# Optimization experiments

Measured on AMD Instinct MI355X. Metric: run time of the kernel, lower is better.

The kernel has to match this reference:

```python
import jax, jax.numpy as jnp
import numpy as np

N = 50000
E = 800000
IN_DIM = 128
HID = 256


def _sage_conv(x, src, dst, W_l, b_l, W_r, num_nodes):
    # PyG SAGEConv (aggr='mean'): out = lin_l(mean_{j in N(i)} x_j) + lin_r(x_i)
    msgs = x[src]                                   # [E, D] gather of source feats
    agg = jax.ops.segment_sum(msgs, dst, num_segments=num_nodes)   # [N, D]
    deg = jax.ops.segment_sum(jnp.ones((src.shape[0],), dtype=x.dtype), dst,
                              num_segments=num_nodes)              # [N]
    agg = agg / jnp.maximum(deg, 1.0)[:, None]      # mean aggregation
    return agg @ W_l + b_l + x @ W_r


def setup_inputs() -> dict:
    key = jax.random.key(0)
    k = jax.random.split(key, 8)
    x = jax.random.normal(k[0], (N, IN_DIM), dtype=jnp.float32)
    edge_index = jax.random.randint(k[1], (2, E), 0, N, dtype=jnp.int64)
    s1 = 1.0 / np.sqrt(IN_DIM)
    s2 = 1.0 / np.sqrt(HID)
    W1_l = jax.random.uniform(k[2], (IN_DIM, HID), jnp.float32, -s1, s1)
    b1 = jax.random.uniform(k[3], (HID,), jnp.float32, -s1, s1)
    W1_r = jax.random.uniform(k[4], (IN_DIM, HID), jnp.float32, -s1, s1)
    W2_l = jax.random.uniform(k[5], (HID, HID), jnp.float32, -s2, s2)
    b2 = jax.random.uniform(k[6], (HID,), jnp.float32, -s2, s2)
    W2_r = jax.random.uniform(k[7], (HID, HID), jnp.float32, -s2, s2)
    return {"x": x, "edge_index": edge_index,
            "W1_l": W1_l, "b1": b1, "W1_r": W1_r,
            "W2_l": W2_l, "b2": b2, "W2_r": W2_r}


def reference(x, edge_index, W1_l, b1, W1_r, W2_l, b2, W2_r):
    src, dst = edge_index[0], edge_index[1]
    h = _sage_conv(x, src, dst, W1_l, b1, W1_r, N)   # [N, HID]
    h = jax.nn.relu(h)
    # dropout is identity in eval mode
    out = _sage_conv(h, src, dst, W2_l, b2, W2_r, N)  # [N, HID]
    return out
```

## Files before the change

### kernel.cpp

```cpp
#include <hip/hip_runtime.h>
#include <hip/hip_bf16.h>


typedef __attribute__((ext_vector_type(8))) short bf16x8;
typedef __attribute__((ext_vector_type(4))) float f32x4;
typedef __attribute__((ext_vector_type(4))) short s16x4;

constexpr int HIDC = 256;

__device__ __forceinline__ short f2bf(float v) {
  __hip_bfloat16 h = __float2bfloat16(v);
  return *reinterpret_cast<short*>(&h);
}
__device__ __forceinline__ float bf2f(short s) {
  unsigned int u = ((unsigned int)(unsigned short)s) << 16;
  float f;
  __builtin_memcpy(&f, &u, 4);
  return f;
}

__device__ __forceinline__ void gll16(const short* g, short* l) {
  __builtin_amdgcn_global_load_lds(
      (const __attribute__((address_space(1))) unsigned int*)g,
      (__attribute__((address_space(3))) unsigned int*)l, 16, 0, 0);
}

__global__ __launch_bounds__(256) void deg_rank_kernel(
    const int* __restrict__ dst, int* __restrict__ deg, int* __restrict__ rank,
    int E, int N) {
  int e = blockIdx.x * blockDim.x + threadIdx.x;
  if (e < E) {
    int d = dst[e];
    if ((unsigned)d < (unsigned)N) rank[e] = atomicAdd(&deg[d], 1);
  }
}

__global__ __launch_bounds__(256) void blocksum_kernel(
    const int* __restrict__ deg, int* __restrict__ bsum, int N) {
  __shared__ int red[256];
  int i = blockIdx.x * 256 + threadIdx.x;
  red[threadIdx.x] = (i < N) ? deg[i] : 0;
  __syncthreads();
#pragma unroll
  for (int off = 128; off > 0; off >>= 1) {
    if (threadIdx.x < off) red[threadIdx.x] += red[threadIdx.x + off];
    __syncthreads();
  }
  if (threadIdx.x == 0) bsum[blockIdx.x] = red[0];
}

__global__ __launch_bounds__(256) void bscan_kernel(
    const int* __restrict__ bsum, int* __restrict__ boff,
    int* __restrict__ row_start, int nb, int N) {
  __shared__ int s[256];
  int t = threadIdx.x;
  s[t] = (t < nb) ? bsum[t] : 0;
  __syncthreads();
  for (int off = 1; off < 256; off <<= 1) {
    int v = (t >= off) ? s[t - off] : 0;
    __syncthreads();
    s[t] += v;
    __syncthreads();
  }
  if (t < nb) boff[t] = (t == 0) ? 0 : s[t - 1];
  if (t == nb - 1) row_start[N] = s[t];
}

__global__ __launch_bounds__(256) void scatter_offsets_kernel(
    const int* __restrict__ deg, const int* __restrict__ boff,
    int* __restrict__ row_start, int N) {
  __shared__ int s[256];
  int i = blockIdx.x * 256 + threadIdx.x;
  int t = threadIdx.x;
  int v = (i < N) ? deg[i] : 0;
  s[t] = v;
  __syncthreads();
  for (int off = 1; off < 256; off <<= 1) {
    int u = (t >= off) ? s[t - off] : 0;
    __syncthreads();
    s[t] += u;
    __syncthreads();
  }
  if (i < N) row_start[i] = s[t] - v + boff[blockIdx.x];
}

__global__ __launch_bounds__(256) void fill2_kernel(
    const int* __restrict__ src, const int* __restrict__ dst,
    const int* __restrict__ rank, const int* __restrict__ row_start,
    int* __restrict__ esrc, int E, int N) {
  int e = blockIdx.x * blockDim.x + threadIdx.x;
  if (e < E) {
    int d = dst[e];
    if ((unsigned)d < (unsigned)N) esrc[row_start[d] + rank[e]] = src[e];
  }
}

__global__ __launch_bounds__(256) void xconv_kernel(
    const float4* __restrict__ x, s16x4* __restrict__ hi,
    s16x4* __restrict__ lo, int total4) {
  int i = blockIdx.x * 256 + threadIdx.x;
  if (i >= total4) return;
  float4 v = x[i];
  s16x4 h, l;
  h.x = f2bf(v.x); l.x = f2bf(v.x - bf2f(h.x));
  h.y = f2bf(v.y); l.y = f2bf(v.y - bf2f(h.y));
  h.z = f2bf(v.z); l.z = f2bf(v.z - bf2f(h.z));
  h.w = f2bf(v.w); l.w = f2bf(v.w - bf2f(h.w));
  hi[i] = h;
  lo[i] = l;
}

template <int K, int NN>
__global__ __launch_bounds__(256) void wconv_kernel(
    const float* __restrict__ W, short* __restrict__ Wt_hi,
    short* __restrict__ Wt_lo) {
  int tid = blockIdx.x * 256 + threadIdx.x;
  if (tid >= K * NN) return;
  int k = tid / NN, n = tid % NN;
  float v = W[tid];
  short hv = f2bf(v);
  Wt_hi[n * K + k] = hv;
  Wt_lo[n * K + k] = f2bf(v - bf2f(hv));
}

__global__ __launch_bounds__(256) void gather1_kernel(
    const short* __restrict__ xhi, const int* __restrict__ row_start,
    const int* __restrict__ esrc, short* __restrict__ ahi,
    short* __restrict__ alo, int N) {
  int gid = (int)(((long long)blockIdx.x * 256 + threadIdx.x) >> 4);
  int l = threadIdx.x & 15;
  if (gid >= N) return;
  int lo_e = row_start[gid], hi_e = row_start[gid + 1];
  float acc[8];
#pragma unroll
  for (int j = 0; j < 8; ++j) acc[j] = 0.f;
  int e = lo_e;
  for (; e + 3 < hi_e; e += 4) {
    bf16x8 v0 = *(const bf16x8*)(xhi + (size_t)esrc[e] * 128 + l * 8);
    bf16x8 v1 = *(const bf16x8*)(xhi + (size_t)esrc[e + 1] * 128 + l * 8);
    bf16x8 v2 = *(const bf16x8*)(xhi + (size_t)esrc[e + 2] * 128 + l * 8);
    bf16x8 v3 = *(const bf16x8*)(xhi + (size_t)esrc[e + 3] * 128 + l * 8);
#pragma unroll
    for (int j = 0; j < 8; ++j)
      acc[j] += (bf2f(v0[j]) + bf2f(v1[j])) + (bf2f(v2[j]) + bf2f(v3[j]));
  }
  for (; e < hi_e; ++e) {
    bf16x8 v0 = *(const bf16x8*)(xhi + (size_t)esrc[e] * 128 + l * 8);
#pragma unroll
    for (int j = 0; j < 8; ++j) acc[j] += bf2f(v0[j]);
  }
  float inv = (hi_e > lo_e) ? 1.0f / (float)(hi_e - lo_e) : 0.0f;
  bf16x8 oh, ol;
#pragma unroll
  for (int j = 0; j < 8; ++j) {
    float v = acc[j] * inv;
    short hv = f2bf(v);
    oh[j] = hv;
    ol[j] = f2bf(v - bf2f(hv));
  }
  *(bf16x8*)(ahi + (size_t)gid * 128 + l * 8) = oh;
  *(bf16x8*)(alo + (size_t)gid * 128 + l * 8) = ol;
}

__global__ __launch_bounds__(256) void gather2_kernel(
    const short* __restrict__ hhi, const int* __restrict__ row_start,
    const int* __restrict__ esrc, short* __restrict__ ahi,
    short* __restrict__ alo, int N) {
  int gid = (int)(((long long)blockIdx.x * 256 + threadIdx.x) >> 5);
  int l = threadIdx.x & 31;
  if (gid >= N) return;
  int lo_e = row_start[gid], hi_e = row_start[gid + 1];
  float acc[8];
#pragma unroll
  for (int j = 0; j < 8; ++j) acc[j] = 0.f;
  int e = lo_e;
  for (; e + 3 < hi_e; e += 4) {
    bf16x8 v0 = *(const bf16x8*)(hhi + (size_t)esrc[e] * HIDC + l * 8);
    bf16x8 v1 = *(const bf16x8*)(hhi + (size_t)esrc[e + 1] * HIDC + l * 8);
    bf16x8 v2 = *(const bf16x8*)(hhi + (size_t)esrc[e + 2] * HIDC + l * 8);
    bf16x8 v3 = *(const bf16x8*)(hhi + (size_t)esrc[e + 3] * HIDC + l * 8);
#pragma unroll
    for (int j = 0; j < 8; ++j)
      acc[j] += (bf2f(v0[j]) + bf2f(v1[j])) + (bf2f(v2[j]) + bf2f(v3[j]));
  }
  for (; e < hi_e; ++e) {
    bf16x8 v0 = *(const bf16x8*)(hhi + (size_t)esrc[e] * HIDC + l * 8);
#pragma unroll
    for (int j = 0; j < 8; ++j) acc[j] += bf2f(v0[j]);
  }
  float inv = (hi_e > lo_e) ? 1.0f / (float)(hi_e - lo_e) : 0.0f;
  bf16x8 oh, ol;
#pragma unroll
  for (int j = 0; j < 8; ++j) {
    float v = acc[j] * inv;
    short hv = f2bf(v);
    oh[j] = hv;
    ol[j] = f2bf(v - bf2f(hv));
  }
  *(bf16x8*)(ahi + (size_t)gid * HIDC + l * 8) = oh;
  *(bf16x8*)(alo + (size_t)gid * HIDC + l * 8) = ol;
}

template <int K1, bool RELU, bool OUTBF>
__global__ __launch_bounds__(256, 4) void mfma_gemm(
    const short* __restrict__ Ahi, const short* __restrict__ Alo,
    const short* __restrict__ Xhi, const short* __restrict__ Xlo,
    const short* __restrict__ WLhi, const short* __restrict__ WLlo,
    const short* __restrict__ WRhi, const short* __restrict__ WRlo,
    const float* __restrict__ bias, float* __restrict__ Cf,
    short* __restrict__ Chi, short* __restrict__ Clo, int M) {
  __shared__ __align__(16) short As_hi[128][32];
  __shared__ __align__(16) short As_lo[128][32];
  __shared__ __align__(16) short Bs_hi[128][32];
  __shared__ __align__(16) short Bs_lo[128][32];

  const int tid = threadIdx.x;
  const int lane = tid & 63;
  const int w = tid >> 6;
  const int brow = blockIdx.x * 128;
  const int bcol = blockIdx.y * 128;
  const int wrl = (w >> 1) * 64;
  const int wcl = (w & 1) * 64;

  const int lrow = lane >> 2;
  const int lc = lane & 3;
  const int r1 = 16 * w + lrow;
  const int r2 = 64 + 16 * w + lrow;
  const int ga1 = min(brow + r1, M - 1);
  const int ga2 = min(brow + r2, M - 1);
  const int sw1 = (lc ^ ((r1 >> 1) & 3)) << 3;
  const int sw2 = (lc ^ ((r2 >> 1) & 3)) << 3;
  const size_t aoff1 = (size_t)ga1 * K1 + sw1;
  const size_t aoff2 = (size_t)ga2 * K1 + sw2;
  const size_t boff1 = (size_t)(bcol + r1) * K1 + sw1;
  const size_t boff2 = (size_t)(bcol + r2) * K1 + sw2;
  short* const lAh1 = &As_hi[16 * w][0];
  short* const lAh2 = &As_hi[64 + 16 * w][0];
  short* const lAl1 = &As_lo[16 * w][0];
  short* const lAl2 = &As_lo[64 + 16 * w][0];
  short* const lBh1 = &Bs_hi[16 * w][0];
  short* const lBh2 = &Bs_hi[64 + 16 * w][0];
  short* const lBl1 = &Bs_lo[16 * w][0];
  short* const lBl2 = &Bs_lo[64 + 16 * w][0];

  f32x4 acc[4][4];
#pragma unroll
  for (int m = 0; m < 4; ++m)
#pragma unroll
    for (int n = 0; n < 4; ++n) acc[m][n] = (f32x4){0.f, 0.f, 0.f, 0.f};

  const int fr = lane & 15;
  const int q = lane >> 4;

  for (int k0 = 0; k0 < 2 * K1; k0 += 32) {
    const bool left = k0 < K1;
    const int kk = left ? k0 : k0 - K1;
    const short* __restrict__ Aph = left ? Ahi : Xhi;
    const short* __restrict__ Apl = left ? Alo : Xlo;
    const short* __restrict__ Bph = left ? WLhi : WRhi;
    const short* __restrict__ Bpl = left ? WLlo : WRlo;

    __syncthreads();
    gll16(Aph + aoff1 + kk, lAh1);
    gll16(Aph + aoff2 + kk, lAh2);
    gll16(Apl + aoff1 + kk, lAl1);
    gll16(Apl + aoff2 + kk, lAl2);
    gll16(Bph + boff1 + kk, lBh1);
    gll16(Bph + boff2 + kk, lBh2);
    gll16(Bpl + boff1 + kk, lBl1);
    gll16(Bpl + boff2 + kk, lBl2);
    __syncthreads();

    bf16x8 bh[4], bl[4];
#pragma unroll
    for (int n = 0; n < 4; ++n) {
      int r = wcl + n * 16 + fr;
      int off = r * 32 + ((q ^ ((r >> 1) & 3)) << 3);
      bh[n] = *(const bf16x8*)(&Bs_hi[0][0] + off);
      bl[n] = *(const bf16x8*)(&Bs_lo[0][0] + off);
    }
#pragma unroll
    for (int m = 0; m < 4; ++m) {
      int r = wrl + m * 16 + fr;
      int off = r * 32 + ((q ^ ((r >> 1) & 3)) << 3);
      bf16x8 ah = *(const bf16x8*)(&As_hi[0][0] + off);
      bf16x8 al = *(const bf16x8*)(&As_lo[0][0] + off);
#pragma unroll
      for (int n = 0; n < 4; ++n) {
        acc[m][n] = __builtin_amdgcn_mfma_f32_16x16x32_bf16(ah, bh[n],
                                                            acc[m][n], 0, 0, 0);
        acc[m][n] = __builtin_amdgcn_mfma_f32_16x16x32_bf16(ah, bl[n],
                                                            acc[m][n], 0, 0, 0);
        acc[m][n] = __builtin_amdgcn_mfma_f32_16x16x32_bf16(al, bh[n],
                                                            acc[m][n], 0, 0, 0);
      }
    }
  }

  const int lcol = lane & 15;
  const int lrw = (lane >> 4) * 4;
#pragma unroll
  for (int m = 0; m < 4; ++m) {
    int gr0 = brow + wrl + m * 16 + lrw;
#pragma unroll
    for (int n = 0; n < 4; ++n) {
      int gc = bcol + wcl + n * 16 + lcol;
      float bv = bias[gc];
#pragma unroll
      for (int j = 0; j < 4; ++j) {
        int gr = gr0 + j;
        if (gr >= M) continue;
        float v = acc[m][n][j] + bv;
        if (RELU) v = fmaxf(v, 0.f);
        if (OUTBF) {
          short hv = f2bf(v);
          Chi[(size_t)gr * HIDC + gc] = hv;
          Clo[(size_t)gr * HIDC + gc] = f2bf(v - bf2f(hv));
        } else {
          Cf[(size_t)gr * HIDC + gc] = v;
        }
      }
    }
  }
}

extern "C" void kernel_launch(void* const* d_in, const int* in_sizes, int n_in,
                              void* d_out, int out_size, void* d_ws,
                              size_t ws_size, hipStream_t stream) {
  const float* x = (const float*)d_in[0];
  const int* ei = (const int*)d_in[1];
  const float* W1l = (const float*)d_in[2];
  const float* b1 = (const float*)d_in[3];
  const float* W1r = (const float*)d_in[4];
  const float* W2l = (const float*)d_in[5];
  const float* b2 = (const float*)d_in[6];
  const float* W2r = (const float*)d_in[7];
  float* out = (float*)d_out;

  const int N = in_sizes[0] / 128;
  const int E = in_sizes[1] / 2;
  const int* src = ei;
  const int* dst = ei + E;

  char* ws = (char*)d_ws;
  size_t off = 0;
  auto walloc = [&](size_t bytes) {
    void* p = ws + off;
    off += (bytes + 255) & ~(size_t)255;
    return p;
  };
  int* deg = (int*)walloc((size_t)N * 4);
  int* row_start = (int*)walloc((size_t)(N + 1) * 4);
  int* rank = (int*)walloc((size_t)E * 4);
  int* esrc = (int*)walloc((size_t)E * 4);
  int* bsum = (int*)walloc(256 * 4);
  int* boff = (int*)walloc(256 * 4);
  short* x_hi = (short*)walloc((size_t)N * 128 * 2);
  short* x_lo = (short*)walloc((size_t)N * 128 * 2);
  short* agg1_hi = (short*)walloc((size_t)N * 128 * 2);
  short* agg1_lo = (short*)walloc((size_t)N * 128 * 2);
  short* h_hi = (short*)walloc((size_t)N * 256 * 2);
  short* h_lo = (short*)walloc((size_t)N * 256 * 2);
  short* agg2_hi = (short*)walloc((size_t)N * 256 * 2);
  short* agg2_lo = (short*)walloc((size_t)N * 256 * 2);
  short* Wt1l_hi = (short*)walloc(128 * 256 * 2);
  short* Wt1l_lo = (short*)walloc(128 * 256 * 2);
  short* Wt1r_hi = (short*)walloc(128 * 256 * 2);
  short* Wt1r_lo = (short*)walloc(128 * 256 * 2);
  short* Wt2l_hi = (short*)walloc(256 * 256 * 2);
  short* Wt2l_lo = (short*)walloc(256 * 256 * 2);
  short* Wt2r_hi = (short*)walloc(256 * 256 * 2);
  short* Wt2r_lo = (short*)walloc(256 * 256 * 2);
  (void)ws_size;
  (void)n_in;
  (void)out_size;

  const int BLK = 256;
  const int eblocks = (E + BLK - 1) / BLK;
  const int nblocks = (N + BLK - 1) / BLK;

  xconv_kernel<<<(N * 32 + BLK - 1) / BLK, BLK, 0, stream>>>(
      (const float4*)x, (s16x4*)x_hi, (s16x4*)x_lo, N * 32);
  wconv_kernel<128, 256><<<(128 * 256 + BLK - 1) / BLK, BLK, 0, stream>>>(
      W1l, Wt1l_hi, Wt1l_lo);
  wconv_kernel<128, 256><<<(128 * 256 + BLK - 1) / BLK, BLK, 0, stream>>>(
      W1r, Wt1r_hi, Wt1r_lo);
  wconv_kernel<256, 256><<<(256 * 256 + BLK - 1) / BLK, BLK, 0, stream>>>(
      W2l, Wt2l_hi, Wt2l_lo);
  wconv_kernel<256, 256><<<(256 * 256 + BLK - 1) / BLK, BLK, 0, stream>>>(
      W2r, Wt2r_hi, Wt2r_lo);

  hipMemsetAsync(deg, 0, (size_t)N * 4, stream);
  deg_rank_kernel<<<eblocks, BLK, 0, stream>>>(dst, deg, rank, E, N);
  blocksum_kernel<<<nblocks, BLK, 0, stream>>>(deg, bsum, N);
  bscan_kernel<<<1, 256, 0, stream>>>(bsum, boff, row_start, nblocks, N);
  scatter_offsets_kernel<<<nblocks, BLK, 0, stream>>>(deg, boff, row_start, N);
  fill2_kernel<<<eblocks, BLK, 0, stream>>>(src, dst, rank, row_start, esrc, E,
                                            N);

  gather1_kernel<<<(N * 16 + BLK - 1) / BLK, BLK, 0, stream>>>(
      x_hi, row_start, esrc, agg1_hi, agg1_lo, N);
  {
    dim3 grid((N + 127) / 128, 2);
    mfma_gemm<128, true, true><<<grid, BLK, 0, stream>>>(
        agg1_hi, agg1_lo, x_hi, x_lo, Wt1l_hi, Wt1l_lo, Wt1r_hi, Wt1r_lo, b1,
        nullptr, h_hi, h_lo, N);
  }

  gather2_kernel<<<(N * 32 + BLK - 1) / BLK, BLK, 0, stream>>>(
      h_hi, row_start, esrc, agg2_hi, agg2_lo, N);
  {
    dim3 grid((N + 127) / 128, 2);
    mfma_gemm<256, false, false><<<grid, BLK, 0, stream>>>(
        agg2_hi, agg2_lo, h_hi, h_lo, Wt2l_hi, Wt2l_lo, Wt2r_hi, Wt2r_lo, b2,
        out, nullptr, nullptr, N);
  }
}
```

Before: 361.8 us.

## Enlarge GEMM row tile to 256 and remap 1D grid for L2 locality

The split-bf16 MFMA GEMM tile grows from 128x128 to 256x128 per block. Each wave now covers 128 rows, so every B fragment loaded from LDS feeds twice as many MFMAs, and B tiles are reloaded from global memory half as often. The 2D grid becomes a 1D grid of 400 blocks that pairs the two column halves of each group of row tiles, so neighbouring blocks share A rows in cache. In exchange, the accumulators double to 128 floats per thread and launch bounds drop to 2 blocks per CU, which lowers occupancy and raises register pressure.

Result: faster. 347.0 us (-4.1%).

```diff
diff --git a/kernel.cpp b/kernel.cpp
--- a/kernel.cpp
+++ b/kernel.cpp
@@ -202,50 +202,50 @@
 }
 
 template <int K1, bool RELU, bool OUTBF>
-__global__ __launch_bounds__(256, 4) void mfma_gemm(
+__global__ __launch_bounds__(256, 2) void mfma_gemm(
     const short* __restrict__ Ahi, const short* __restrict__ Alo,
     const short* __restrict__ Xhi, const short* __restrict__ Xlo,
     const short* __restrict__ WLhi, const short* __restrict__ WLlo,
     const short* __restrict__ WRhi, const short* __restrict__ WRlo,
     const float* __restrict__ bias, float* __restrict__ Cf,
     short* __restrict__ Chi, short* __restrict__ Clo, int M) {
-  __shared__ __align__(16) short As_hi[128][32];
-  __shared__ __align__(16) short As_lo[128][32];
+  __shared__ __align__(16) short As_hi[256][32];
+  __shared__ __align__(16) short As_lo[256][32];
   __shared__ __align__(16) short Bs_hi[128][32];
   __shared__ __align__(16) short Bs_lo[128][32];
+
+  const int g = blockIdx.x;
+  const int p = 8 * (g >> 4) + (g & 7);
+  const int bcolb = (g >> 3) & 1;
+  if (p >= 196) return;
+  const int brow = p * 256;
+  const int bcol = bcolb * 128;
 
   const int tid = threadIdx.x;
   const int lane = tid & 63;
   const int w = tid >> 6;
-  const int brow = blockIdx.x * 128;
-  const int bcol = blockIdx.y * 128;
-  const int wrl = (w >> 1) * 64;
+  const int wrl = (w >> 1) * 128;
   const int wcl = (w & 1) * 64;
 
   const int lrow = lane >> 2;
   const int lc = lane & 3;
-  const int r1 = 16 * w + lrow;
-  const int r2 = 64 + 16 * w + lrow;
-  const int ga1 = min(brow + r1, M - 1);
-  const int ga2 = min(brow + r2, M - 1);
-  const int sw1 = (lc ^ ((r1 >> 1) & 3)) << 3;
-  const int sw2 = (lc ^ ((r2 >> 1) & 3)) << 3;
-  const size_t aoff1 = (size_t)ga1 * K1 + sw1;
-  const size_t aoff2 = (size_t)ga2 * K1 + sw2;
-  const size_t boff1 = (size_t)(bcol + r1) * K1 + sw1;
-  const size_t boff2 = (size_t)(bcol + r2) * K1 + sw2;
-  short* const lAh1 = &As_hi[16 * w][0];
-  short* const lAh2 = &As_hi[64 + 16 * w][0];
-  short* const lAl1 = &As_lo[16 * w][0];
-  short* const lAl2 = &As_lo[64 + 16 * w][0];
-  short* const lBh1 = &Bs_hi[16 * w][0];
-  short* const lBh2 = &Bs_hi[64 + 16 * w][0];
-  short* const lBl1 = &Bs_lo[16 * w][0];
-  short* const lBl2 = &Bs_lo[64 + 16 * w][0];
-
-  f32x4 acc[4][4];
-#pragma unroll
-  for (int m = 0; m < 4; ++m)
+  size_t aoff[4];
+  size_t boff[2];
+#pragma unroll
+  for (int pp = 0; pp < 4; ++pp) {
+    int r = pp * 64 + 16 * w + lrow;
+    int gr = min(brow + r, M - 1);
+    aoff[pp] = (size_t)gr * K1 + ((lc ^ ((r >> 1) & 3)) << 3);
+  }
+#pragma unroll
+  for (int pp = 0; pp < 2; ++pp) {
+    int r = pp * 64 + 16 * w + lrow;
+    boff[pp] = (size_t)(bcol + r) * K1 + ((lc ^ ((r >> 1) & 3)) << 3);
+  }
+
+  f32x4 acc[8][4];
+#pragma unroll
+  for (int m = 0; m < 8; ++m)
 #pragma unroll
     for (int n = 0; n < 4; ++n) acc[m][n] = (f32x4){0.f, 0.f, 0.f, 0.f};
 
@@ -261,14 +261,16 @@
     const short* __restrict__ Bpl = left ? WLlo : WRlo;
 
     __syncthreads();
-    gll16(Aph + aoff1 + kk, lAh1);
-    gll16(Aph + aoff2 + kk, lAh2);
-    gll16(Apl + aoff1 + kk, lAl1);
-    gll16(Apl + aoff2 + kk, lAl2);
-    gll16(Bph + boff1 + kk, lBh1);
-    gll16(Bph + boff2 + kk, lBh2);
-    gll16(Bpl + boff1 + kk, lBl1);
-    gll16(Bpl + boff2 + kk, lBl2);
+#pragma unroll
+    for (int pp = 0; pp < 4; ++pp) {
+      gll16(Aph + aoff[pp] + kk, &As_hi[pp * 64 + 16 * w][0]);
+      gll16(Apl + aoff[pp] + kk, &As_lo[pp * 64 + 16 * w][0]);
+    }
+#pragma unroll
+    for (int pp = 0; pp < 2; ++pp) {
+      gll16(Bph + boff[pp] + kk, &Bs_hi[pp * 64 + 16 * w][0]);
+      gll16(Bpl + boff[pp] + kk, &Bs_lo[pp * 64 + 16 * w][0]);
+    }
     __syncthreads();
 
     bf16x8 bh[4], bl[4];
@@ -280,7 +282,7 @@
       bl[n] = *(const bf16x8*)(&Bs_lo[0][0] + off);
     }
 #pragma unroll
-    for (int m = 0; m < 4; ++m) {
+    for (int m = 0; m < 8; ++m) {
       int r = wrl + m * 16 + fr;
       int off = r * 32 + ((q ^ ((r >> 1) & 3)) << 3);
       bf16x8 ah = *(const bf16x8*)(&As_hi[0][0] + off);
@@ -300,7 +302,7 @@
   const int lcol = lane & 15;
   const int lrw = (lane >> 4) * 4;
 #pragma unroll
-  for (int m = 0; m < 4; ++m) {
+  for (int m = 0; m < 8; ++m) {
     int gr0 = brow + wrl + m * 16 + lrw;
 #pragma unroll
     for (int n = 0; n < 4; ++n) {
@@ -401,8 +403,7 @@
   gather1_kernel<<<(N * 16 + BLK - 1) / BLK, BLK, 0, stream>>>(
       x_hi, row_start, esrc, agg1_hi, agg1_lo, N);
   {
-    dim3 grid((N + 127) / 128, 2);
-    mfma_gemm<128, true, true><<<grid, BLK, 0, stream>>>(
+    mfma_gemm<128, true, true><<<400, BLK, 0, stream>>>(
         agg1_hi, agg1_lo, x_hi, x_lo, Wt1l_hi, Wt1l_lo, Wt1r_hi, Wt1r_lo, b1,
         nullptr, h_hi, h_lo, N);
   }
@@ -410,8 +411,7 @@
   gather2_kernel<<<(N * 32 + BLK - 1) / BLK, BLK, 0, stream>>>(
       h_hi, row_start, esrc, agg2_hi, agg2_lo, N);
   {
-    dim3 grid((N + 127) / 128, 2);
-    mfma_gemm<256, false, false><<<grid, BLK, 0, stream>>>(
+    mfma_gemm<256, false, false><<<400, BLK, 0, stream>>>(
         agg2_hi, agg2_lo, h_hi, h_lo, Wt2l_hi, Wt2l_lo, Wt2r_hi, Wt2r_lo, b2,
         out, nullptr, nullptr, N);
   }
```
